# Performance work log

Measured on AMD Instinct MI355X. Metric: run time of the kernel, lower is better.

## Reference

```python
import jax, jax.numpy as jnp
import numpy as np

H = 16          # num heads
BUCKETS = 256   # position_buckets -> pos_ebd_size (att_span)
MAX_REL = 512   # max_relative_positions


def _log_bucket(rel, bucket_size, max_position):
    mid = bucket_size // 2
    sign = jnp.sign(rel).astype(jnp.float32)
    abs_pos = jnp.where((rel < mid) & (rel > -mid), mid - 1, jnp.abs(rel)).astype(jnp.float32)
    log_pos = jnp.ceil(jnp.log(abs_pos / mid) / np.log((max_position - 1) / mid) * (mid - 1)) + mid
    bucket = jnp.where(abs_pos <= mid, rel.astype(jnp.float32), log_pos * sign)
    return bucket.astype(jnp.int32)


def _rel_pos(seq_len):
    ids = jnp.arange(seq_len)
    rel = ids[:, None] - ids[None, :]
    return _log_bucket(rel, BUCKETS, MAX_REL)  # [S,S] int32 in [-span, span]


def setup_inputs() -> dict:
    key = jax.random.key(0)
    ks = jax.random.split(key, 16)
    B, S, D = 4, 1024, 1024
    K2 = 2 * BUCKETS
    s = 0.02
    def lin(k, din, dout):
        return jax.random.normal(k, (din, dout), jnp.float32) * s
    return {
        "hidden_states": jax.random.normal(ks[0], (B, S, D), jnp.float32),
        "Wq": lin(ks[1], D, D), "bq": jnp.zeros((D,), jnp.float32),
        "Wk": lin(ks[2], D, D), "bk": jnp.zeros((D,), jnp.float32),
        "Wv": lin(ks[3], D, D), "bv": jnp.zeros((D,), jnp.float32),
        "Wo": lin(ks[4], D, D), "bo": jnp.zeros((D,), jnp.float32),
        "rel_emb": jax.random.normal(ks[5], (K2, D), jnp.float32) * s,
        "ln_g": jnp.ones((D,), jnp.float32), "ln_b": jnp.zeros((D,), jnp.float32),
        "Wpk": lin(ks[6], D, D), "bpk": jnp.zeros((D,), jnp.float32),
        "Wpq": lin(ks[7], D, D), "bpq": jnp.zeros((D,), jnp.float32),
    }


def reference(hidden_states, Wq, bq, Wk, bk, Wv, bv, Wo, bo,
              rel_emb, ln_g, ln_b, Wpk, bpk, Wpq, bpq):
    B, S, D = hidden_states.shape
    hd = D // H
    span = BUCKETS

    def shape_heads(x):  # [*, L, D] -> [*, H, L, hd]
        return x.reshape(*x.shape[:-1], H, hd).swapaxes(-2, -3)

    q = shape_heads(hidden_states @ Wq + bq)  # [B,H,S,hd]
    k = shape_heads(hidden_states @ Wk + bk)
    v = shape_heads(hidden_states @ Wv + bv)

    scale_factor = 3  # 1 + c2p + p2c
    scores = jnp.einsum('bhsd,bhkd->bhsk', q, k) / jnp.sqrt(jnp.float32(hd * scale_factor))

    # relative embeddings: LayerNorm over feature dim
    mu = rel_emb.mean(-1, keepdims=True)
    var = rel_emb.var(-1, keepdims=True)
    re = (rel_emb - mu) / jnp.sqrt(var + 1e-5) * ln_g + ln_b  # [2K, D]

    pos_k = shape_heads(re @ Wpk + bpk)  # [H, 2K, hd]
    pos_q = shape_heads(re @ Wpq + bpq)  # [H, 2K, hd]

    rel = _rel_pos(S)  # [S,S]
    bias_scale = jnp.sqrt(jnp.float32(hd * 2))

    # content-to-position
    c2p = jnp.einsum('bhsd,hkd->bhsk', q, pos_k)  # [B,H,S,2K]
    c2p_idx = jnp.clip(rel + span, 0, 2 * span - 1)  # [S,S]
    c2p = jnp.take_along_axis(c2p, jnp.broadcast_to(c2p_idx[None, None], (B, H, S, S)), axis=-1)
    scores = scores + c2p / bias_scale

    # position-to-content
    p2c = jnp.einsum('bhsd,hkd->bhsk', k, pos_q)  # [B,H,S,2K]
    p2c_idx = jnp.clip(-rel + span, 0, 2 * span - 1)
    p2c = jnp.take_along_axis(p2c, jnp.broadcast_to(p2c_idx[None, None], (B, H, S, S)), axis=-1)
    scores = scores + p2c.swapaxes(-1, -2) / bias_scale

    probs = jax.nn.softmax(scores.astype(jnp.float32), axis=-1).astype(q.dtype)
    ctx = jnp.einsum('bhsk,bhkd->bhsd', probs, v)  # [B,H,S,hd]
    ctx = ctx.swapaxes(1, 2).reshape(B, S, D)
    return ctx @ Wo + bo
```

## Files before the change

kernel.cpp:

```cpp
#include <hip/hip_runtime.h>

typedef unsigned short u16;
typedef __attribute__((ext_vector_type(8))) short short8_t;
typedef __attribute__((ext_vector_type(4))) float floatx4;

typedef const void __attribute__((address_space(1)))* gas_ptr;
typedef void __attribute__((address_space(3)))* las_ptr;

__device__ __forceinline__ float bf2f(u16 u){
  union { unsigned i; float f; } v; v.i = ((unsigned)u) << 16; return v.f;
}
__device__ __forceinline__ u16 f2bf(float x){
  unsigned u = __float_as_uint(x);
  return (u16)((u + 0x7FFFu + ((u >> 16) & 1u)) >> 16);
}
__device__ __forceinline__ int bucket_idx(int delta){
  int b;
  if (delta >= -128 && delta <= 128) b = delta;
  else {
    float a = (float)(delta < 0 ? -delta : delta);
    float lp = ceilf(logf(a * (1.0f / 128.0f)) / logf(511.0f / 128.0f) * 127.0f) + 128.0f;
    b = (int)lp;
    if (delta < 0) b = -b;
  }
  int idx = b + 256;
  return idx < 0 ? 0 : (idx > 511 ? 511 : idx);
}
__device__ __forceinline__ int win_lo(int s0, int t){
  int dlo = s0 - t * 64 - 63;
  int lo = bucket_idx(dlo) & ~1;
  return lo > 384 ? 384 : lo;
}

__global__ __launch_bounds__(256) void k_prep(
    const float* __restrict__ hs,
    const float* __restrict__ W0, const float* __restrict__ W1, const float* __restrict__ W2,
    const float* __restrict__ W3, const float* __restrict__ W4, const float* __restrict__ W5,
    const float* __restrict__ rel, const float* __restrict__ lng, const float* __restrict__ lnb,
    const float* __restrict__ bq, const float* __restrict__ bk, const float* __restrict__ bv,
    const float* __restrict__ bpk, const float* __restrict__ bpq,
    u16* __restrict__ h_bf, u16* __restrict__ Wt5, u16* __restrict__ Wo_t,
    u16* __restrict__ re_bf, u16* __restrict__ idxt,
    float* __restrict__ qkvb, float* __restrict__ posb)
{
  __shared__ float t[64][65];
  const int bid = blockIdx.x, tid = threadIdx.x;
  if (bid < 4096){
    int i = bid * 256 + tid;
    float4 v = ((const float4*)hs)[i];
    ushort4 o;
    o.x = f2bf(v.x); o.y = f2bf(v.y); o.z = f2bf(v.z); o.w = f2bf(v.w);
    ((ushort4*)h_bf)[i] = o;
  } else if (bid < 5632){
    int b2 = bid - 4096;
    int z = b2 >> 8, rem = b2 & 255;
    const float* W = (z == 0) ? W0 : (z == 1) ? W1 : (z == 2) ? W2 : (z == 3) ? W3 : (z == 4) ? W4 : W5;
    u16* Wt = (z < 5) ? (Wt5 + (long)z * 1048576) : Wo_t;
    int n0 = (rem & 15) * 64, k0 = (rem >> 4) * 64;
    #pragma unroll
    for (int i = 0; i < 16; i++){
      int e = i * 256 + tid; int r = e >> 6, c = e & 63;
      t[r][c] = W[(long)(k0 + r) * 1024 + n0 + c];
    }
    __syncthreads();
    #pragma unroll
    for (int i = 0; i < 16; i++){
      int e = i * 256 + tid; int r = e >> 6, c = e & 63;
      Wt[(long)(n0 + r) * 1024 + k0 + c] = f2bf(t[c][r]);
    }
  } else if (bid < 6144){
    int row = bid - 5632;
    float* red = (float*)t;
    float4 v = ((const float4*)(rel + (long)row * 1024))[tid];
    float s  = v.x + v.y + v.z + v.w;
    float s2 = v.x*v.x + v.y*v.y + v.z*v.z + v.w*v.w;
    #pragma unroll
    for (int o = 1; o < 64; o <<= 1){ s += __shfl_xor(s, o); s2 += __shfl_xor(s2, o); }
    if ((tid & 63) == 0){ red[(tid >> 6) * 2] = s; red[(tid >> 6) * 2 + 1] = s2; }
    __syncthreads();
    s  = red[0] + red[2] + red[4] + red[6];
    s2 = red[1] + red[3] + red[5] + red[7];
    float mu  = s * (1.f / 1024.f);
    float var = s2 * (1.f / 1024.f) - mu * mu;
    float rs  = rsqrtf(var + 1e-5f);
    float4 gg = ((const float4*)lng)[tid];
    float4 bb = ((const float4*)lnb)[tid];
    ushort4 o;
    o.x = f2bf((v.x - mu) * rs * gg.x + bb.x);
    o.y = f2bf((v.y - mu) * rs * gg.y + bb.y);
    o.z = f2bf((v.z - mu) * rs * gg.z + bb.z);
    o.w = f2bf((v.w - mu) * rs * gg.w + bb.w);
    ((ushort4*)(re_bf + (long)row * 1024))[tid] = o;
  } else {
    for (int i = tid; i < 2048; i += 256)
      idxt[i] = (u16)bucket_idx(i - 1024);
    for (int i = tid; i < 1024; i += 256){
      qkvb[i] = bq[i]; qkvb[1024 + i] = bk[i]; qkvb[2048 + i] = bv[i];
      posb[i] = bpk[i]; posb[1024 + i] = bpq[i];
    }
  }
}

template<int MODE>
__global__ __launch_bounds__(256) void k_gemm(
    const u16* __restrict__ A, const u16* __restrict__ Bt,
    const float* __restrict__ bias, void* __restrict__ C, void* __restrict__ C2,
    int M, int N, int K, int lda, int ldb,
    const u16* __restrict__ Apos, const float* __restrict__ biaspos, void* __restrict__ Cpos)
{
  __shared__ __attribute__((aligned(16))) u16 smem[16384];
  u16* As = smem;
  u16* Bs = smem + 8192;
  const int bx = blockIdx.x, by = blockIdx.y;
  const int z = blockIdx.z;
  const u16* Ab = A;
  const u16* Bb = Bt;
  const float* biasv = bias;
  bool pospath = false;
  int pz = 0;
  int m0, n0;
  if (MODE == 5){
    if (by >= 32){
      if (bx >= 16) return;
      pospath = true;
      pz = bx >> 3;
      Ab = Apos;
      Bb = Bt + 3145728 + (long)pz * 1048576;
      biasv = biaspos + (pz << 10);
      m0 = (by - 32) * 128;
      n0 = (bx & 7) * 128;
    } else {
      int bid = by * 24 + bx;
      int nf = (bid & 7) * 96 + (bid >> 3);
      m0 = (nf / 24) * 128;
      n0 = (nf % 24) * 128;
    }
  } else if (MODE == 0){
    int bid = by * 8 + bx;
    int nf = (bid & 7) * 32 + (bid >> 3);
    m0 = (nf >> 3) * 128;
    n0 = (nf & 7) * 128;
  } else {
    if (MODE == 4){ Ab = A + (long)z * 65536; Bb = Bt + (long)(z >> 6) * 524288 + (long)(z & 15) * 32768; }
    m0 = by * 128;
    n0 = bx * 128;
  }
  const int tid = threadIdx.x, lane = tid & 63, w = tid >> 6;
  const int wm = (w >> 1) * 64, wn = (w & 1) * 64;
  floatx4 acc[4][4];
  #pragma unroll
  for (int i = 0; i < 4; i++)
    #pragma unroll
    for (int j = 0; j < 4; j++) acc[i][j] = (floatx4){0.f, 0.f, 0.f, 0.f};

  const int r8 = lane >> 3;
  const int cswz = ((lane & 7) ^ r8) << 4;

  for (int kt = 0; kt < K; kt += 64){
    #pragma unroll
    for (int c = 0; c < 4; c++){
      int row = (c * 4 + w) * 8 + r8;
      const char* ga = (const char*)(Ab + (long)(m0 + row) * lda + kt) + cswz;
      __builtin_amdgcn_global_load_lds((gas_ptr)ga, (las_ptr)((char*)As + (c * 4 + w) * 1024), 16, 0, 0);
      const char* gb = (const char*)(Bb + (long)(n0 + row) * ldb + kt) + cswz;
      __builtin_amdgcn_global_load_lds((gas_ptr)gb, (las_ptr)((char*)Bs + (c * 4 + w) * 1024), 16, 0, 0);
    }
    __syncthreads();
    short8_t af[2][4], bfr[2][4];
    #pragma unroll
    for (int kk = 0; kk < 2; kk++){
      #pragma unroll
      for (int i = 0; i < 4; i++){
        int ra = wm + i * 16 + (lane & 15);
        af[kk][i] = *(const short8_t*)((const char*)As + ra * 128 + ((kk * 64 + ((lane >> 4) << 4)) ^ ((ra & 7) << 4)));
        int rb = wn + i * 16 + (lane & 15);
        bfr[kk][i] = *(const short8_t*)((const char*)Bs + rb * 128 + ((kk * 64 + ((lane >> 4) << 4)) ^ ((rb & 7) << 4)));
      }
    }
    #pragma unroll
    for (int i = 0; i < 4; i++)
      #pragma unroll
      for (int j = 0; j < 4; j++){
        acc[i][j] = __builtin_amdgcn_mfma_f32_16x16x32_bf16(af[0][i], bfr[0][j], acc[i][j], 0, 0, 0);
        acc[i][j] = __builtin_amdgcn_mfma_f32_16x16x32_bf16(af[1][i], bfr[1][j], acc[i][j], 0, 0, 0);
      }
    __syncthreads();
  }

  if (MODE == 0){
    float* fs = (float*)smem;
    #pragma unroll
    for (int h = 0; h < 2; h++){
      if ((w & 1) == h){
        #pragma unroll
        for (int i = 0; i < 4; i++)
          #pragma unroll
          for (int j = 0; j < 4; j++)
            #pragma unroll
            for (int r = 0; r < 4; r++){
              int ml = wm + i * 16 + ((lane >> 4) << 2) + r;
              int nl = j * 16 + (lane & 15);
              fs[ml * 64 + (nl ^ (((ml >> 2) & 3) << 4))] = acc[i][j][r] + biasv[n0 + h * 64 + nl];
            }
      }
      __syncthreads();
      const int row16 = tid >> 4, cch = tid & 15;
      #pragma unroll
      for (int rr = 0; rr < 8; rr++){
        int ml = rr * 16 + row16;
        float4 vv = *(const float4*)&fs[ml * 64 + ((cch * 4) ^ (((ml >> 2) & 3) << 4))];
        *(float4*)((float*)C + (long)(m0 + ml) * N + n0 + h * 64 + cch * 4) = vv;
      }
      __syncthreads();
    }
    return;
  }

  if (MODE == 4){
    #pragma unroll
    for (int i = 0; i < 4; i++){
      #pragma unroll
      for (int j = 0; j < 4; j++){
        #pragma unroll
        for (int r = 0; r < 4; r++){
          int ml = wm + i * 16 + ((lane >> 4) << 2) + r;
          int nl = wn + j * 16 + (lane & 15);
          int byte_ = ml * 256 + ((nl * 2) ^ ((ml & 7) << 4));
          *(u16*)((char*)smem + byte_) = f2bf(exp2f(acc[i][j][r] * 0.12751743f));
        }
      }
    }
    __syncthreads();
    const int row16 = tid >> 4, cch = tid & 15;
    #pragma unroll
    for (int rr = 0; rr < 8; rr++){
      int ml = rr * 16 + row16;
      short8_t vv = *(const short8_t*)((const char*)smem + ml * 256 + ((cch * 16) ^ ((ml & 7) << 4)));
      *(short8_t*)((u16*)C + (long)z * 524288 + (long)(m0 + ml) * 512 + n0 + cch * 8) = vv;
    }
    return;
  }

  if (MODE == 5){
    if (pospath){
      #pragma unroll
      for (int i = 0; i < 4; i++){
        #pragma unroll
        for (int j = 0; j < 4; j++){
          #pragma unroll
          for (int r = 0; r < 4; r++){
            int m = m0 + wm + i * 16 + ((lane >> 4) << 2) + r;
            int n = n0 + wn + j * 16 + (lane & 15);
            float v = acc[i][j][r] + biasv[n];
            ((u16*)Cpos)[(long)pz * 524288 + ((long)(n >> 6) * 512 + m) * 64 + (n & 63)] = f2bf(v);
          }
        }
      }
      return;
    }
    if (n0 >= 2048){
      #pragma unroll
      for (int i = 0; i < 4; i++){
        #pragma unroll
        for (int j = 0; j < 4; j++){
          #pragma unroll
          for (int r = 0; r < 4; r++){
            int ml = wm + i * 16 + ((lane >> 4) << 2) + r;
            int nl = wn + j * 16 + (lane & 15);
            float v = acc[i][j][r] + biasv[n0 + nl];
            int byte_ = nl * 256 + ((ml * 2) ^ ((nl & 7) << 4));
            *(u16*)((char*)smem + byte_) = f2bf(v);
          }
        }
      }
      __syncthreads();
      #pragma unroll
      for (int rr = 0; rr < 8; rr++){
        int nl = rr * 16 + (tid >> 4);
        int np = n0 + nl - 2048;
        int mc = tid & 15;
        short8_t vv = *(const short8_t*)((const char*)smem + nl * 256 + ((mc * 16) ^ ((nl & 7) << 4)));
        int m = m0 + mc * 8;
        long base = ((long)((m >> 10) * 16 + (np >> 6)) * 64 + (np & 63)) * 1024 + (m & 1023);
        *(short8_t*)((u16*)C2 + base) = vv;
      }
    } else {
      #pragma unroll
      for (int i = 0; i < 4; i++){
        #pragma unroll
        for (int j = 0; j < 4; j++){
          #pragma unroll
          for (int r = 0; r < 4; r++){
            int ml = wm + i * 16 + ((lane >> 4) << 2) + r;
            int nl = wn + j * 16 + (lane & 15);
            float v = acc[i][j][r] + biasv[n0 + nl];
            int byte_ = ml * 256 + ((nl * 2) ^ ((ml & 7) << 4));
            *(u16*)((char*)smem + byte_) = f2bf(v);
          }
        }
      }
      __syncthreads();
      const int row16 = tid >> 4, cch = tid & 15;
      const int mat = n0 >> 10;
      u16* Cd = (u16*)C + (long)mat * 4194304;
      #pragma unroll
      for (int rr = 0; rr < 8; rr++){
        int ml = rr * 16 + row16;
        short8_t vv = *(const short8_t*)((const char*)smem + ml * 256 + ((cch * 16) ^ ((ml & 7) << 4)));
        int m = m0 + ml;
        int np = (n0 & 1023) + cch * 8;
        long base = ((long)((m >> 10) * 16 + (np >> 6)) * 1024 + (m & 1023)) * 64 + (np & 63);
        *(short8_t*)(Cd + base) = vv;
      }
    }
    return;
  }
}

__global__ __launch_bounds__(256, 2) void k_bias(
    const u16* __restrict__ EC, const u16* __restrict__ EP,
    const u16* __restrict__ T3, u16* __restrict__ EB, int bhbase)
{
  __shared__ __attribute__((aligned(16))) u16 C2W[2][8192];
  __shared__ __attribute__((aligned(16))) u16 P2W[2][8192];
  __shared__ __attribute__((aligned(16))) u16 IDW[2][128];
  const int flat0 = blockIdx.x;
  const int chunk = gridDim.x >> 3;
  const int flat = (flat0 & 7) * chunk + (flat0 >> 3);
  const int bhl = flat >> 5;
  const int sb  = (flat >> 1) & 15;
  const int kq  = flat & 1;
  const int bh = bhbase + bhl;
  const int tid = threadIdx.x, lane = tid & 63, w = tid >> 6;
  const int s0 = sb * 64;
  const u16* c2b = EC + (long)bh * 524288;
  const u16* p2b = EP + (long)bh * 524288;
  u16* EBb = EB + ((long)bhl << 20);

  const int r2 = tid >> 2;
  const int q2 = tid & 3;
  const int c2key = (r2 & 15) << 4;

  auto STAGE = [&](int buf, int t){
    const int ixlo = win_lo(s0, t);
    const int k0 = t * 64;
    #pragma unroll
    for (int r = 0; r < 16; r++){
      int row = w * 16 + r;
      const char* sa = (const char*)(c2b + (long)(s0 + row) * 512 + ixlo) + ((lane * 4) ^ ((row & 15) << 4));
      __builtin_amdgcn_global_load_lds((gas_ptr)sa, (las_ptr)((char*)&C2W[buf][0] + row * 256), 4, 0, 0);
      const char* sp = (const char*)(p2b + (long)(k0 + row) * 512 + ixlo) + ((lane * 4) ^ ((row & 15) << 4));
      __builtin_amdgcn_global_load_lds((gas_ptr)sp, (las_ptr)((char*)&P2W[buf][0] + row * 256), 4, 0, 0);
    }
    if (w == 3){
      int dev = s0 - k0 - 64;
      __builtin_amdgcn_global_load_lds((gas_ptr)((const char*)(T3 + (dev + 1024)) + lane * 4),
                                       (las_ptr)((char*)&IDW[buf][0]), 4, 0, 0);
    }
  };

  const int t0 = kq * 8;
  STAGE(0, t0);
  asm volatile("s_waitcnt vmcnt(0)" ::: "memory");
  __builtin_amdgcn_s_barrier();

  for (int i = 0; i < 8; i++){
    const int t = t0 + i, buf = i & 1;
    const int k0 = t * 64;
    const int ixlo = win_lo(s0, t);

    if (i < 7) STAGE(buf ^ 1, t + 1);

    u16 ov[16];
    #pragma unroll
    for (int c = 0; c < 16; c++){
      int kl = q2 * 16 + c;
      int j = r2 - kl + 64;
      int ix = (int)IDW[buf][j];
      int x = (ix - ixlo) * 2;
      float b1 = bf2f(*(const u16*)((const char*)&C2W[buf][0] + r2 * 256 + (x ^ c2key)));
      float b2 = bf2f(*(const u16*)((const char*)&P2W[buf][0] + kl * 256 + (x ^ ((kl & 15) << 4))));
      ov[c] = f2bf(b1 * b2);
    }
    u16* dst = EBb + (((long)(s0 + r2)) << 10) + k0 + q2 * 16;
    uint4 st0, st1;
    st0.x = (unsigned)ov[0]  | ((unsigned)ov[1]  << 16);
    st0.y = (unsigned)ov[2]  | ((unsigned)ov[3]  << 16);
    st0.z = (unsigned)ov[4]  | ((unsigned)ov[5]  << 16);
    st0.w = (unsigned)ov[6]  | ((unsigned)ov[7]  << 16);
    st1.x = (unsigned)ov[8]  | ((unsigned)ov[9]  << 16);
    st1.y = (unsigned)ov[10] | ((unsigned)ov[11] << 16);
    st1.z = (unsigned)ov[12] | ((unsigned)ov[13] << 16);
    st1.w = (unsigned)ov[14] | ((unsigned)ov[15] << 16);
    *(uint4*)dst = st0;
    *(uint4*)(dst + 8) = st1;

    if (i < 7){
      asm volatile("s_waitcnt vmcnt(2)" ::: "memory");
      __builtin_amdgcn_s_barrier();
    }
  }
}

__global__ __launch_bounds__(256, 3) void k_attn_eb(
    const u16* __restrict__ Q, const u16* __restrict__ K, const u16* __restrict__ Vt,
    const u16* __restrict__ EB, u16* __restrict__ ctx, int bhbase)
{
  __shared__ __attribute__((aligned(16))) u16 Ks[2][4096];
  __shared__ __attribute__((aligned(16))) u16 Vs[2][4096];
  __shared__ __attribute__((aligned(16))) u16 EBs[4096];
  __shared__ __attribute__((aligned(16))) u16 Pt[4096];
  const int flat0 = blockIdx.x;
  const int chunk = gridDim.x >> 3;
  const int flat = (flat0 & 7) * chunk + (flat0 >> 3);
  const int bhl = flat >> 4, sb = flat & 15;
  const int bh = bhbase + bhl;
  const int tid = threadIdx.x, lane = tid & 63, w = tid >> 6;
  const int s15 = lane & 15, g = lane >> 4;
  const int s0 = sb * 64;
  const int myrow = w * 16 + s15;
  const int s_row = s0 + myrow;
  const u16* Qb  = Q   + (long)bh * 65536;
  const u16* Kg  = K   + (long)bh * 65536;
  const u16* Vg  = Vt  + (long)bh * 65536;
  const u16* EBg = EB  + ((long)bhl << 20);

  short8_t qf0 = *(const short8_t*)(Qb + (long)s_row * 64 + g * 8);
  short8_t qf1 = *(const short8_t*)(Qb + (long)s_row * 64 + 32 + g * 8);

  const int srow8  = lane >> 3;
  const int schunk = (lane & 7) ^ srow8;
  const float sA2 = 0.10411754f;

  auto STAGE_KV = [&](int buf, int kt){
    #pragma unroll
    for (int ii = 0; ii < 2; ii++){
      int i = w * 2 + ii;
      int row = i * 8 + srow8;
      __builtin_amdgcn_global_load_lds(
        (gas_ptr)((const char*)(Kg + (long)(kt + row) * 64) + schunk * 16),
        (las_ptr)((char*)&Ks[buf][0] + i * 1024), 16, 0, 0);
      __builtin_amdgcn_global_load_lds(
        (gas_ptr)((const char*)(Vg + (long)row * 1024 + kt) + schunk * 16),
        (las_ptr)((char*)&Vs[buf][0] + i * 1024), 16, 0, 0);
    }
  };
  auto STAGE_EB = [&](int kt){
    #pragma unroll
    for (int ii = 0; ii < 2; ii++){
      int rowl = w * 16 + ii * 8 + srow8;
      const char* src = (const char*)(EBg + (((long)(s0 + rowl)) << 10) + kt) + schunk * 16;
      __builtin_amdgcn_global_load_lds((gas_ptr)src,
        (las_ptr)((char*)EBs + (w * 2 + ii) * 1024), 16, 0, 0);
    }
  };

  STAGE_KV(0, 0);
  STAGE_EB(0);

  float rowsum = 0.f;
  floatx4 oacc[4];
  #pragma unroll
  for (int dt = 0; dt < 4; dt++) oacc[dt] = (floatx4){0.f, 0.f, 0.f, 0.f};

  const int psw = (myrow & 7) << 4;

  for (int t = 0; t < 16; t++){
    const int buf = t & 1;
    const int kt = t * 64;

    asm volatile("s_waitcnt vmcnt(2)" ::: "memory");
    asm volatile("s_waitcnt lgkmcnt(0)" ::: "memory");
    __builtin_amdgcn_s_barrier();

    STAGE_KV(buf ^ 1, (t < 15) ? kt + 64 : 0);

    floatx4 a[4];
    #pragma unroll
    for (int T = 0; T < 4; T++){
      int row = T * 16 + s15;
      const char* rp = (const char*)&Ks[buf][0] + row * 128;
      int sw = (row & 7) << 4;
      short8_t k0v = *(const short8_t*)(rp + ((g * 16) ^ sw));
      short8_t k1v = *(const short8_t*)(rp + ((64 + g * 16) ^ sw));
      floatx4 acc = (floatx4){0.f, 0.f, 0.f, 0.f};
      acc = __builtin_amdgcn_mfma_f32_16x16x32_bf16(k0v, qf0, acc, 0, 0, 0);
      acc = __builtin_amdgcn_mfma_f32_16x16x32_bf16(k1v, qf1, acc, 0, 0, 0);
      a[T] = acc;
    }

    asm volatile("s_waitcnt vmcnt(4)" ::: "memory");

    #pragma unroll
    for (int T = 0; T < 4; T++){
      uint2 ebv = *(const uint2*)((const char*)EBs + myrow * 128 + ((T * 32 + g * 8) ^ psw));
      float e0 = exp2f(a[T][0] * sA2) * bf2f((u16)(ebv.x & 0xffff));
      float e1 = exp2f(a[T][1] * sA2) * bf2f((u16)(ebv.x >> 16));
      float e2 = exp2f(a[T][2] * sA2) * bf2f((u16)(ebv.y & 0xffff));
      float e3 = exp2f(a[T][3] * sA2) * bf2f((u16)(ebv.y >> 16));
      u16 p0 = f2bf(e0), p1 = f2bf(e1), p2v = f2bf(e2), p3 = f2bf(e3);
      rowsum += (bf2f(p0) + bf2f(p1)) + (bf2f(p2v) + bf2f(p3));
      uint2 pk2;
      pk2.x = (unsigned)p0  | ((unsigned)p1 << 16);
      pk2.y = (unsigned)p2v | ((unsigned)p3 << 16);
      *(uint2*)((char*)Pt + myrow * 128 + ((T * 32 + g * 8) ^ psw)) = pk2;
    }

    asm volatile("s_waitcnt lgkmcnt(0)" ::: "memory");
    STAGE_EB((t < 15) ? kt + 64 : 0);

    #pragma unroll
    for (int M = 0; M < 2; M++){
      short8_t pf = *(const short8_t*)((const char*)Pt + myrow * 128 + ((M * 64 + g * 16) ^ psw));
      #pragma unroll
      for (int dt = 0; dt < 4; dt++){
        int drow = dt * 16 + s15;
        short8_t vf = *(const short8_t*)((const char*)&Vs[buf][0] + drow * 128 + ((M * 64 + g * 16) ^ ((drow & 7) << 4)));
        oacc[dt] = __builtin_amdgcn_mfma_f32_16x16x32_bf16(pf, vf, oacc[dt], 0, 0, 0);
      }
    }
  }

  asm volatile("s_waitcnt vmcnt(0)" ::: "memory");

  rowsum += __shfl_xor(rowsum, 16);
  rowsum += __shfl_xor(rowsum, 32);
  float rinv = 1.f / rowsum;

  const int b = bh >> 4, h = bh & 15;
  #pragma unroll
  for (int r = 0; r < 4; r++){
    float ri = __shfl(rinv, g * 4 + r);
    int s_out = s0 + w * 16 + g * 4 + r;
    #pragma unroll
    for (int dt = 0; dt < 4; dt++){
      long oi = ((long)b * 1024 + s_out) * 1024 + h * 64 + dt * 16 + s15;
      ctx[oi] = f2bf(oacc[dt][r] * ri);
    }
  }
}

extern "C" void kernel_launch(void* const* d_in, const int* in_sizes, int n_in,
                              void* d_out, int out_size, void* d_ws, size_t ws_size,
                              hipStream_t stream){
  const float* hs  = (const float*)d_in[0];
  const float* Wq  = (const float*)d_in[1];
  const float* bq  = (const float*)d_in[2];
  const float* Wk  = (const float*)d_in[3];
  const float* bk  = (const float*)d_in[4];
  const float* Wv  = (const float*)d_in[5];
  const float* bv  = (const float*)d_in[6];
  const float* Wo  = (const float*)d_in[7];
  const float* bo  = (const float*)d_in[8];
  const float* rel = (const float*)d_in[9];
  const float* lng = (const float*)d_in[10];
  const float* lnb = (const float*)d_in[11];
  const float* Wpk = (const float*)d_in[12];
  const float* bpk = (const float*)d_in[13];
  const float* Wpq = (const float*)d_in[14];
  const float* bpq = (const float*)d_in[15];

  char* ws = (char*)d_ws;
  size_t off = 0;
  auto alloc = [&](size_t bytes){ size_t o = off; off += (bytes + 255) & ~(size_t)255; return o; };
  u16* Wo_t  = (u16*)(ws + alloc(1048576UL * 2));
  u16* Qd    = (u16*)(ws + alloc(4194304UL * 2));
  u16* Kd    = (u16*)(ws + alloc(4194304UL * 2));
  u16* Vtd   = (u16*)(ws + alloc(4194304UL * 2));
  u16* ECd   = (u16*)(ws + alloc(33554432UL * 2));
  u16* EPd   = (u16*)(ws + alloc(33554432UL * 2));
  u16* ctx   = (u16*)(ws + alloc(4194304UL * 2));
  u16* idxt  = (u16*)(ws + alloc(2048UL * 2));
  float* qkvb = (float*)(ws + alloc(3072UL * 4));
  float* posb = (float*)(ws + alloc(2048UL * 4));
  size_t dead0 = off;
  u16* h_bf  = (u16*)(ws + alloc(4194304UL * 2));
  u16* Wt5   = (u16*)(ws + alloc(5UL * 1048576 * 2));
  u16* re_bf = (u16*)(ws + alloc(524288UL * 2));
  u16* posk  = (u16*)(ws + alloc(524288UL * 2));
  u16* posq  = (u16*)(ws + alloc(524288UL * 2));
  u16* EB    = (u16*)(ws + dead0);
  const bool full = (ws_size >= dead0 + 134217728UL);
  (void)posq; (void)Kd;

  k_prep<<<6145, 256, 0, stream>>>(hs, Wq, Wk, Wv, Wpk, Wpq, Wo, rel, lng, lnb,
                                   bq, bk, bv, bpk, bpq,
                                   h_bf, Wt5, Wo_t, re_bf, idxt, qkvb, posb);

  k_gemm<5><<<dim3(24, 36, 1), 256, 0, stream>>>(h_bf, Wt5, qkvb, Qd, Vtd,
                                                 4096, 3072, 1024, 1024, 1024,
                                                 re_bf, posb, posk);
  k_gemm<4><<<dim3(4, 8, 128), 256, 0, stream>>>(Qd, posk, nullptr, ECd, nullptr,
                                                 1024, 512, 64, 64, 64,
                                                 nullptr, nullptr, nullptr);

  if (full){
    k_bias   <<<dim3(2048), 256, 0, stream>>>(ECd, EPd, idxt, EB, 0);
    k_attn_eb<<<dim3(1024), 256, 0, stream>>>(Qd, Kd, Vtd, EB, ctx, 0);
  } else {
    k_bias   <<<dim3(1024), 256, 0, stream>>>(ECd, EPd, idxt, EB, 0);
    k_attn_eb<<<dim3(512),  256, 0, stream>>>(Qd, Kd, Vtd, EB, ctx, 0);
    k_bias   <<<dim3(1024), 256, 0, stream>>>(ECd, EPd, idxt, EB, 32);
    k_attn_eb<<<dim3(512),  256, 0, stream>>>(Qd, Kd, Vtd, EB, ctx, 32);
  }

  k_gemm<0><<<dim3(8, 32, 1), 256, 0, stream>>>(ctx, Wo_t, bo, d_out, nullptr,
                                                4096, 1024, 1024, 1024, 1024,
                                                nullptr, nullptr, nullptr);
}
```

Baseline: 258.8 us.

## Double-buffer GEMM LDS tiles with async prefetch and regroup XCD tile mapping

Switches the GEMM kernel to dynamic shared memory with two LDS stages. It prefetches the next K tile via global_load_lds while the current one is computed, using vmcnt waits and raw barriers in place of __syncthreads. It also changes the block-to-tile mapping in the fused QKV GEMM so each XCD covers a contiguous 2D patch, aiming for better L2 reuse. The cost is double the LDS per block (64KB), which may lower occupancy, and reliance on exact vmcnt counting.

```diff
diff --git a/kernel.cpp b/kernel.cpp
--- a/kernel.cpp
+++ b/kernel.cpp
@@ -108,9 +108,7 @@
     int M, int N, int K, int lda, int ldb,
     const u16* __restrict__ Apos, const float* __restrict__ biaspos, void* __restrict__ Cpos)
 {
-  __shared__ __attribute__((aligned(16))) u16 smem[16384];
-  u16* As = smem;
-  u16* Bs = smem + 8192;
+  extern __shared__ __attribute__((aligned(16))) u16 smem[];
   const int bx = blockIdx.x, by = blockIdx.y;
   const int z = blockIdx.z;
   const u16* Ab = A;
@@ -131,9 +129,10 @@
       n0 = (bx & 7) * 128;
     } else {
       int bid = by * 24 + bx;
-      int nf = (bid & 7) * 96 + (bid >> 3);
-      m0 = (nf / 24) * 128;
-      n0 = (nf % 24) * 128;
+      int xcd = bid & 7, r = bid >> 3;
+      int cm = xcd >> 1, cn = xcd & 1;
+      m0 = (cm * 8 + r / 12) * 128;
+      n0 = (cn * 12 + r % 12) * 128;
     }
   } else if (MODE == 0){
     int bid = by * 8 + bx;
@@ -156,7 +155,9 @@
   const int r8 = lane >> 3;
   const int cswz = ((lane & 7) ^ r8) << 4;
 
-  for (int kt = 0; kt < K; kt += 64){
+  auto STAGE = [&](int buf, int kt){
+    u16* As = smem + buf * 16384;
+    u16* Bs = As + 8192;
     #pragma unroll
     for (int c = 0; c < 4; c++){
       int row = (c * 4 + w) * 8 + r8;
@@ -165,7 +166,10 @@
       const char* gb = (const char*)(Bb + (long)(n0 + row) * ldb + kt) + cswz;
       __builtin_amdgcn_global_load_lds((gas_ptr)gb, (las_ptr)((char*)Bs + (c * 4 + w) * 1024), 16, 0, 0);
     }
-    __syncthreads();
+  };
+  auto COMPUTE = [&](int buf){
+    const u16* As = smem + buf * 16384;
+    const u16* Bs = As + 8192;
     short8_t af[2][4], bfr[2][4];
     #pragma unroll
     for (int kk = 0; kk < 2; kk++){
@@ -184,7 +188,26 @@
         acc[i][j] = __builtin_amdgcn_mfma_f32_16x16x32_bf16(af[0][i], bfr[0][j], acc[i][j], 0, 0, 0);
         acc[i][j] = __builtin_amdgcn_mfma_f32_16x16x32_bf16(af[1][i], bfr[1][j], acc[i][j], 0, 0, 0);
       }
+  };
+
+  if (MODE == 4){
+    STAGE(0, 0);
     __syncthreads();
+    COMPUTE(0);
+    __syncthreads();
+  } else {
+    const int T = K >> 6;
+    STAGE(0, 0);
+    STAGE(1, 64);
+    for (int t = 0; t < T; t++){
+      const int buf = t & 1;
+      if (t < T - 1) asm volatile("s_waitcnt vmcnt(8)" ::: "memory");
+      else           asm volatile("s_waitcnt vmcnt(0)" ::: "memory");
+      __builtin_amdgcn_s_barrier();
+      COMPUTE(buf);
+      __builtin_amdgcn_s_barrier();
+      if (t < T - 2) STAGE(buf, (t + 2) << 6);
+    }
   }
 
   if (MODE == 0){
@@ -587,12 +610,12 @@
                                    bq, bk, bv, bpk, bpq,
                                    h_bf, Wt5, Wo_t, re_bf, idxt, qkvb, posb);
 
-  k_gemm<5><<<dim3(24, 36, 1), 256, 0, stream>>>(h_bf, Wt5, qkvb, Qd, Vtd,
-                                                 4096, 3072, 1024, 1024, 1024,
-                                                 re_bf, posb, posk);
-  k_gemm<4><<<dim3(4, 8, 128), 256, 0, stream>>>(Qd, posk, nullptr, ECd, nullptr,
-                                                 1024, 512, 64, 64, 64,
-                                                 nullptr, nullptr, nullptr);
+  k_gemm<5><<<dim3(24, 36, 1), 256, 65536, stream>>>(h_bf, Wt5, qkvb, Qd, Vtd,
+                                                     4096, 3072, 1024, 1024, 1024,
+                                                     re_bf, posb, posk);
+  k_gemm<4><<<dim3(4, 8, 128), 256, 32768, stream>>>(Qd, posk, nullptr, ECd, nullptr,
+                                                     1024, 512, 64, 64, 64,
+                                                     nullptr, nullptr, nullptr);
 
   if (full){
     k_bias   <<<dim3(2048), 256, 0, stream>>>(ECd, EPd, idxt, EB, 0);
@@ -604,7 +627,7 @@
     k_attn_eb<<<dim3(512),  256, 0, stream>>>(Qd, Kd, Vtd, EB, ctx, 32);
   }
 
-  k_gemm<0><<<dim3(8, 32, 1), 256, 0, stream>>>(ctx, Wo_t, bo, d_out, nullptr,
-                                                4096, 1024, 1024, 1024, 1024,
-                                                nullptr, nullptr, nullptr);
-}
+  k_gemm<0><<<dim3(8, 32, 1), 256, 65536, stream>>>(ctx, Wo_t, bo, d_out, nullptr,
+                                                    4096, 1024, 1024, 1024, 1024,
+                                                    nullptr, nullptr, nullptr);
+}
```

Result: faster. 238.6 us (-7.8%).
